# Performance work log

Measured on AMD Instinct MI355X. Metric: run time of the kernel, lower is better.

The kernel has to match this reference:

```python
import jax, jax.numpy as jnp
import numpy as np
from functools import partial

B, L, D = 4, 1024, 512
H = 8                 # attention heads
DIN = 2 * D           # mamba d_inner (expand=2)
N = 16                # mamba d_state
K = 4                 # mamba d_conv
R = 32                # dt_rank = ceil(D/16)


def setup_inputs() -> dict:
    key = jax.random.key(0)
    ks = jax.random.split(key, 24)
    s = 0.02
    nrm = lambda k, sh: (jax.random.normal(k, sh, dtype=jnp.float32) * s)
    inp = {
        'x':       jax.random.normal(ks[0], (B, L, D), dtype=jnp.float32),
        # attention projections
        'Wq': nrm(ks[1], (D, D)), 'bq': jnp.zeros((D,), jnp.float32),
        'Wk': nrm(ks[2], (D, D)), 'bk': jnp.zeros((D,), jnp.float32),
        'Wv': nrm(ks[3], (D, D)), 'bv': jnp.zeros((D,), jnp.float32),
        'Wo': nrm(ks[4], (D, D)), 'bo': jnp.zeros((D,), jnp.float32),
        # layernorms
        'ln1_g': jnp.ones((D,), jnp.float32), 'ln1_b': jnp.zeros((D,), jnp.float32),
        'ln2_g': jnp.ones((D,), jnp.float32), 'ln2_b': jnp.zeros((D,), jnp.float32),
        # mamba params
        'm_Win':   nrm(ks[5], (D, 2 * DIN)),            # in_proj (no bias)
        'm_conv_w': nrm(ks[6], (DIN, 1, K)),            # depthwise causal conv
        'm_conv_b': jnp.zeros((DIN,), jnp.float32),
        'm_Wx':    nrm(ks[7], (DIN, R + 2 * N)),        # x_proj (no bias)
        'm_Wdt':   nrm(ks[8], (R, DIN)),                # dt_proj
        'm_bdt':   jnp.full((DIN,), 0.5, jnp.float32),
        'm_Alog':  jnp.log(jnp.broadcast_to(jnp.arange(1, N + 1, dtype=jnp.float32), (DIN, N))).copy(),
        'm_D':     jnp.ones((DIN,), jnp.float32),
        'm_Wout':  nrm(ks[9], (DIN, D)),                # out_proj (no bias)
    }
    return inp


def _layernorm(x, g, b, eps=1e-5):
    mu = jnp.mean(x, axis=-1, keepdims=True)
    var = jnp.var(x, axis=-1, keepdims=True)
    return (x - mu) * jax.lax.rsqrt(var + eps) * g + b


def _mamba(x, Win, conv_w, conv_b, Wx, Wdt, bdt, Alog, Dp, Wout):
    b, l, _ = x.shape
    xz = x @ Win                           # [B,L,2*DIN]
    xi, z = xz[..., :DIN], xz[..., DIN:]
    # causal depthwise conv over time
    xt = jnp.transpose(xi, (0, 2, 1))      # [B,DIN,L]
    xt = jax.lax.conv_general_dilated(
        xt, conv_w, window_strides=(1,), padding=[(K - 1, 0)],
        feature_group_count=DIN, dimension_numbers=('NCH', 'OIH', 'NCH'))
    xc = jax.nn.silu(jnp.transpose(xt, (0, 2, 1)) + conv_b)   # [B,L,DIN]
    # input-dependent SSM params
    dbl = xc @ Wx                          # [B,L,R+2N]
    dt = jax.nn.softplus(dbl[..., :R] @ Wdt + bdt)            # [B,L,DIN]
    Bm = dbl[..., R:R + N]                 # [B,L,N]
    Cm = dbl[..., R + N:]                  # [B,L,N]
    A = -jnp.exp(Alog)                     # [DIN,N]
    dA = jnp.exp(dt[..., None] * A)                     # [B,L,DIN,N]
    dBx = (dt * xc)[..., None] * Bm[:, :, None, :]      # [B,L,DIN,N]

    def step(h, t):
        dA_t, dBx_t, C_t = t
        h = h * dA_t + dBx_t               # [B,DIN,N]
        y = jnp.einsum('bdn,bn->bd', h, C_t)
        return h, y

    h0 = jnp.zeros((b, DIN, N), xc.dtype)
    _, ys = jax.lax.scan(step, h0, (jnp.swapaxes(dA, 0, 1),
                                    jnp.swapaxes(dBx, 0, 1),
                                    jnp.swapaxes(Cm, 0, 1)))
    y = jnp.swapaxes(ys, 0, 1)             # [B,L,DIN]
    y = y + xc * Dp
    y = y * jax.nn.silu(z)
    return y @ Wout                        # [B,L,D]


def reference(x, Wq, bq, Wk, bk, Wv, bv, Wo, bo, ln1_g, ln1_b, ln2_g, ln2_b,
              m_Win, m_conv_w, m_conv_b, m_Wx, m_Wdt, m_bdt, m_Alog, m_D, m_Wout):
    b, l, d = x.shape
    E = d // H
    q = (x @ Wq + bq).reshape(b, l, H, E)
    k = (x @ Wk + bk).reshape(b, l, H, E)
    v = (x @ Wv + bv).reshape(b, l, H, E)
    scores = jnp.einsum('blhe,bshe->bhls', q, k) * (E ** -0.5)
    attn = jax.nn.softmax(scores, axis=-1)                    # [B,H,L,L]
    o = jnp.einsum('bhls,bshe->blhe', attn, v).reshape(b, l, d)
    new_x = o @ Wo + bo
    x1 = _layernorm(x + new_x, ln1_g, ln1_b)
    y = _mamba(x1, m_Win, m_conv_w, m_conv_b, m_Wx, m_Wdt, m_bdt, m_Alog, m_D, m_Wout)
    out = _layernorm(x1 + y, ln2_g, ln2_b)
    return out, attn
```

## Files before the change

### kernel.cpp

```cpp
#include <hip/hip_runtime.h>
#include <hip/hip_bf16.h>

#define BB 4
#define LL 1024
#define DD 512
#define HH 8
#define EE 64
#define DIN 1024
#define NN 16
#define KK 4
#define RR 32
#define BL (BB*LL)
#define CC 32
#define LC (LL/CC)
#define BDN (BB*DIN*NN)

using bf16 = __hip_bfloat16;
typedef __attribute__((ext_vector_type(8))) short short8;
typedef __attribute__((ext_vector_type(4))) float f32x4;

__device__ __forceinline__ float ldf(const float* p) { return *p; }
__device__ __forceinline__ float ldf(const bf16* p) { return __bfloat162float(*p); }
__device__ __forceinline__ void stf(float* p, float v) { *p = v; }
__device__ __forceinline__ void stf(bf16* p, float v) { *p = __float2bfloat16(v); }

__global__ void cvt_k(const float* __restrict__ in, bf16* __restrict__ out, int n)
{
    int i = blockIdx.x * 256 + threadIdx.x;
    if (i < n) out[i] = __float2bfloat16(in[i]);
}

struct TpwJob { const float* in; bf16* out; int Kd, Nd, gx, tile0; };
struct TpwJobs { TpwJob j[7]; };

__global__ void tpw_batch_k(TpwJobs jobs)
{
    const int tile = blockIdx.x;
    int ji = 0;
#pragma unroll
    for (int i = 1; i < 7; ++i) if (tile >= jobs.j[i].tile0) ji = i;
    const TpwJob jb = jobs.j[ji];
    const int lt = tile - jb.tile0;
    const int n0 = (lt % jb.gx) * 32;
    const int k0 = (lt / jb.gx) * 32;

    __shared__ float t[32][33];
    const int tx = threadIdx.x & 31, ty = threadIdx.x >> 5;
#pragma unroll
    for (int i = 0; i < 4; ++i)
        t[ty + 8 * i][tx] = jb.in[(size_t)(k0 + ty + 8 * i) * jb.Nd + n0 + tx];
    __syncthreads();
#pragma unroll
    for (int i = 0; i < 4; ++i)
        jb.out[(size_t)(n0 + ty + 8 * i) * jb.Kd + k0 + tx] = __float2bfloat16(t[tx][ty + 8 * i]);
}

__global__ void tpv_k(const bf16* __restrict__ v, bf16* __restrict__ vT)
{
    __shared__ float t[32][33];
    const int l0 = blockIdx.x * 32;
    const int e0 = blockIdx.y * 32;
    const int bh = blockIdx.z, b = bh >> 3, h = bh & 7;
    const int tx = threadIdx.x & 31, ty = threadIdx.x >> 5;
#pragma unroll
    for (int i = 0; i < 4; ++i)
        t[ty + 8 * i][tx] = ldf(&v[(size_t)(b * LL + l0 + ty + 8 * i) * DD + h * EE + e0 + tx]);
    __syncthreads();
#pragma unroll
    for (int i = 0; i < 4; ++i)
        stf(&vT[(size_t)(bh * EE + e0 + ty + 8 * i) * LL + l0 + tx], t[tx][ty + 8 * i]);
}

template <typename TC>
__global__ void mfma_gemm128_k(const bf16* __restrict__ A, int lda,
                               const bf16* __restrict__ Bt0, size_t bstride, int ldb,
                               const float* __restrict__ bias0,
                               const float* __restrict__ bias1,
                               const float* __restrict__ bias2,
                               TC* __restrict__ C0, size_t cstride, int ldc, int Kd)
{
    const int z = blockIdx.z;
    const bf16* Bt = Bt0 + (size_t)z * bstride;
    TC* C = C0 + (size_t)z * cstride;
    const float* bias = (z == 0) ? bias0 : (z == 1) ? bias1 : bias2;

    const int lane = threadIdx.x & 63;
    const int w = threadIdx.x >> 6;
    const int m = lane & 15, quad = lane >> 4;
    const int m0 = blockIdx.y * 128 + (w >> 1) * 64;
    const int n0 = blockIdx.x * 128 + (w & 1) * 64;

    f32x4 acc[4][4] = {};
    const bf16* ap = A + (size_t)(m0 + m) * lda + quad * 8;
    const bf16* bp = Bt + (size_t)(n0 + m) * ldb + quad * 8;
    const size_t rsa = (size_t)16 * lda;
    const size_t rsb = (size_t)16 * ldb;
    for (int k = 0; k < Kd; k += 32) {
        short8 a[4], b[4];
#pragma unroll
        for (int i = 0; i < 4; ++i) a[i] = *(const short8*)(ap + i * rsa + k);
#pragma unroll
        for (int j = 0; j < 4; ++j) b[j] = *(const short8*)(bp + j * rsb + k);
#pragma unroll
        for (int i = 0; i < 4; ++i)
#pragma unroll
            for (int j = 0; j < 4; ++j)
                acc[i][j] = __builtin_amdgcn_mfma_f32_16x16x32_bf16(a[i], b[j], acc[i][j], 0, 0, 0);
    }
    float bv[4];
#pragma unroll
    for (int j = 0; j < 4; ++j) bv[j] = bias ? bias[n0 + j * 16 + m] : 0.f;
#pragma unroll
    for (int i = 0; i < 4; ++i)
#pragma unroll
        for (int j = 0; j < 4; ++j)
#pragma unroll
            for (int r = 0; r < 4; ++r) {
                int row = m0 + i * 16 + quad * 4 + r;
                int col = n0 + j * 16 + m;
                stf(&C[(size_t)row * ldc + col], acc[i][j][r] + bv[j]);
            }
}

template <typename TC>
__global__ void mfma_gemm_k(const bf16* __restrict__ A, int lda,
                            const bf16* __restrict__ Bt, int ldb,
                            const float* __restrict__ bias,
                            TC* __restrict__ C, int ldc, int Kd)
{
    const int lane = threadIdx.x & 63;
    const int w = threadIdx.x >> 6;
    const int m = lane & 15, quad = lane >> 4;
    const int m0 = blockIdx.y * 64 + (w >> 1) * 32;
    const int n0 = blockIdx.x * 64 + (w & 1) * 32;
    f32x4 acc[2][2] = {};
    const bf16* a0p = A + (size_t)(m0 + m) * lda + quad * 8;
    const bf16* a1p = a0p + (size_t)16 * lda;
    const bf16* b0p = Bt + (size_t)(n0 + m) * ldb + quad * 8;
    const bf16* b1p = b0p + (size_t)16 * ldb;
    for (int k = 0; k < Kd; k += 32) {
        short8 a0 = *(const short8*)(a0p + k);
        short8 a1 = *(const short8*)(a1p + k);
        short8 b0 = *(const short8*)(b0p + k);
        short8 b1 = *(const short8*)(b1p + k);
        acc[0][0] = __builtin_amdgcn_mfma_f32_16x16x32_bf16(a0, b0, acc[0][0], 0, 0, 0);
        acc[0][1] = __builtin_amdgcn_mfma_f32_16x16x32_bf16(a0, b1, acc[0][1], 0, 0, 0);
        acc[1][0] = __builtin_amdgcn_mfma_f32_16x16x32_bf16(a1, b0, acc[1][0], 0, 0, 0);
        acc[1][1] = __builtin_amdgcn_mfma_f32_16x16x32_bf16(a1, b1, acc[1][1], 0, 0, 0);
    }
#pragma unroll
    for (int i = 0; i < 2; ++i)
#pragma unroll
        for (int j = 0; j < 2; ++j)
#pragma unroll
            for (int r = 0; r < 4; ++r) {
                int row = m0 + i * 16 + quad * 4 + r;
                int col = n0 + j * 16 + (lane & 15);
                float vv = acc[i][j][r] + (bias ? bias[col] : 0.f);
                stf(&C[(size_t)row * ldc + col], vv);
            }
}

__global__ void attn_fused_k(const bf16* __restrict__ q, const bf16* __restrict__ k,
                             const bf16* __restrict__ vT,
                             float* __restrict__ attn, bf16* __restrict__ o)
{
    const int rt = blockIdx.x;
    const int bh = blockIdx.y, b = bh >> 3, h = bh & 7;
    const int w = threadIdx.x >> 6;
    const int lane = threadIdx.x & 63;
    const int m = lane & 15, quad = lane >> 4;
    __shared__ float pm[4][16], ps[4][16];
    __shared__ bf16 P[16][1032];

    const bf16* qp = q + (size_t)(b * LL + rt * 16 + m) * DD + h * EE + quad * 8;
    short8 a0 = *(const short8*)(qp);
    short8 a1 = *(const short8*)(qp + 32);

    f32x4 acc[16];
#pragma unroll
    for (int t = 0; t < 16; ++t) {
        int srow = w * 256 + t * 16 + m;
        const bf16* kp = k + (size_t)(b * LL + srow) * DD + h * EE + quad * 8;
        short8 b0 = *(const short8*)(kp);
        short8 b1 = *(const short8*)(kp + 32);
        f32x4 c = {};
        c = __builtin_amdgcn_mfma_f32_16x16x32_bf16(a0, b0, c, 0, 0, 0);
        c = __builtin_amdgcn_mfma_f32_16x16x32_bf16(a1, b1, c, 0, 0, 0);
        acc[t] = c;
    }

#pragma unroll
    for (int r = 0; r < 4; ++r) {
        float mx = -1e30f;
#pragma unroll
        for (int t = 0; t < 16; ++t) { acc[t][r] *= 0.125f; mx = fmaxf(mx, acc[t][r]); }
        mx = fmaxf(mx, __shfl_xor(mx, 1)); mx = fmaxf(mx, __shfl_xor(mx, 2));
        mx = fmaxf(mx, __shfl_xor(mx, 4)); mx = fmaxf(mx, __shfl_xor(mx, 8));
        if (m == 0) pm[w][quad * 4 + r] = mx;
    }
    __syncthreads();
#pragma unroll
    for (int r = 0; r < 4; ++r) {
        float mx = fmaxf(fmaxf(pm[0][quad * 4 + r], pm[1][quad * 4 + r]),
                         fmaxf(pm[2][quad * 4 + r], pm[3][quad * 4 + r]));
        float s = 0.f;
#pragma unroll
        for (int t = 0; t < 16; ++t) { float e = __expf(acc[t][r] - mx); acc[t][r] = e; s += e; }
        s += __shfl_xor(s, 1); s += __shfl_xor(s, 2);
        s += __shfl_xor(s, 4); s += __shfl_xor(s, 8);
        if (m == 0) ps[w][quad * 4 + r] = s;
    }
    __syncthreads();
#pragma unroll
    for (int r = 0; r < 4; ++r) {
        float tot = ps[0][quad * 4 + r] + ps[1][quad * 4 + r] + ps[2][quad * 4 + r] + ps[3][quad * 4 + r];
        float inv = 1.f / tot;
        int row = rt * 16 + quad * 4 + r;
        float* op = attn + ((size_t)bh * LL + row) * LL + w * 256 + (lane & 15);
#pragma unroll
        for (int t = 0; t < 16; ++t) {
            float pv = acc[t][r] * inv;
            op[t * 16] = pv;
            P[quad * 4 + r][w * 256 + t * 16 + m] = __float2bfloat16(pv);
        }
    }
    __syncthreads();

    const bf16* vp = vT + (size_t)(bh * EE + w * 16 + m) * LL + quad * 8;
    f32x4 oacc = {};
    for (int k0 = 0; k0 < LL; k0 += 32) {
        short8 af = *(const short8*)(&P[m][k0 + quad * 8]);
        short8 bf = *(const short8*)(vp + k0);
        oacc = __builtin_amdgcn_mfma_f32_16x16x32_bf16(af, bf, oacc, 0, 0, 0);
    }
#pragma unroll
    for (int r = 0; r < 4; ++r) {
        int row = rt * 16 + quad * 4 + r;
        stf(&o[(size_t)(b * LL + row) * DD + h * EE + w * 16 + (lane & 15)], oacc[r]);
    }
}

template <typename TA, typename TC, bool SP>
__global__ void gemm_k(const TA* __restrict__ A, int lda,
                       const float* __restrict__ B, int ldb,
                       const float* __restrict__ bias,
                       TC* __restrict__ C, int ldc,
                       int M, int N, int Kd)
{
    __shared__ float As[32][33];
    __shared__ float Bs[32][33];
    const int tid = threadIdx.x;
    const int tx = tid & 31;
    const int ty = tid >> 5;
    const int rowBase = blockIdx.y * 32;
    const int colBase = blockIdx.x * 32;
    float acc[4] = {0.f, 0.f, 0.f, 0.f};

    for (int k0 = 0; k0 < Kd; k0 += 32) {
#pragma unroll
        for (int i = 0; i < 4; ++i) {
            int r = ty + 8 * i;
            As[r][tx] = ldf(&A[(size_t)(rowBase + r) * lda + k0 + tx]);
            Bs[r][tx] = B[(size_t)(k0 + r) * ldb + colBase + tx];
        }
        __syncthreads();
#pragma unroll 8
        for (int kk = 0; kk < 32; ++kk) {
            float bv = Bs[kk][tx];
#pragma unroll
            for (int i = 0; i < 4; ++i) acc[i] += As[ty + 8 * i][kk] * bv;
        }
        __syncthreads();
    }
#pragma unroll
    for (int i = 0; i < 4; ++i) {
        int row = rowBase + ty + 8 * i;
        int col = colBase + tx;
        float r = acc[i] + (bias ? bias[col] : 0.f);
        if (SP) r = (r > 20.f) ? r : log1pf(__expf(r));
        stf(&C[(size_t)row * ldc + col], r);
    }
}

template <typename TA, typename TR, typename TO>
__global__ void add_ln_k(const TA* __restrict__ a, const TR* __restrict__ r,
                         const float* __restrict__ g, const float* __restrict__ be,
                         TO* __restrict__ out)
{
    const int row = blockIdx.x;
    const int tid = threadIdx.x;
    __shared__ float red[256];
    const size_t base = (size_t)row * DD;
    float v0 = ldf(&a[base + tid]) + ldf(&r[base + tid]);
    float v1 = ldf(&a[base + 256 + tid]) + ldf(&r[base + 256 + tid]);
    red[tid] = v0 + v1;
    __syncthreads();
    for (int off = 128; off > 0; off >>= 1) {
        if (tid < off) red[tid] += red[tid + off];
        __syncthreads();
    }
    const float mu = red[0] * (1.f / 512.f);
    __syncthreads();
    float d0 = v0 - mu, d1 = v1 - mu;
    red[tid] = d0 * d0 + d1 * d1;
    __syncthreads();
    for (int off = 128; off > 0; off >>= 1) {
        if (tid < off) red[tid] += red[tid + off];
        __syncthreads();
    }
    const float rs = rsqrtf(red[0] * (1.f / 512.f) + 1e-5f);
    stf(&out[base + tid], d0 * rs * g[tid] + be[tid]);
    stf(&out[base + 256 + tid], d1 * rs * g[tid + 256] + be[tid + 256]);
}

__global__ void conv_silu_k(const bf16* __restrict__ xz,
                            const float* __restrict__ w,
                            const float* __restrict__ cb,
                            bf16* __restrict__ xc)
{
    const int idx = blockIdx.x * 256 + threadIdx.x;
    const int c = idx & (DIN - 1);
    const int t = (idx >> 10) & (LL - 1);
    const int b = idx >> 20;
    float acc = cb[c];
    const bf16* xi = xz + (size_t)b * LL * (2 * DIN) + c;
#pragma unroll
    for (int j = 0; j < KK; ++j) {
        int tt = t - (KK - 1) + j;
        if (tt >= 0) acc += w[c * KK + j] * ldf(&xi[(size_t)tt * (2 * DIN)]);
    }
    stf(&xc[idx], acc / (1.f + __expf(-acc)));
}

__global__ void scan_p1_k(const bf16* __restrict__ dt, const bf16* __restrict__ xc,
                          const float* __restrict__ dbl, const float* __restrict__ Alog,
                          float* __restrict__ P, float* __restrict__ S)
{
    const int d = (blockIdx.x & 3) * 256 + threadIdx.x;
    const int c = blockIdx.x >> 2;
    const int b = blockIdx.y;
    float A[NN];
#pragma unroll
    for (int n = 0; n < NN; ++n) A[n] = -__expf(Alog[d * NN + n]);
    const int t0 = c * LC;
    const bf16* dt_b = dt + ((size_t)b * LL + t0) * DIN + d;
    const bf16* xc_b = xc + ((size_t)b * LL + t0) * DIN + d;
    const float* dbl_b = dbl + ((size_t)b * LL + t0) * 64 + RR;
    float h[NN];
#pragma unroll
    for (int n = 0; n < NN; ++n) h[n] = 0.f;
    float sdt = 0.f;
#pragma unroll 4
    for (int t = 0; t < LC; ++t) {
        float dtv = ldf(&dt_b[(size_t)t * DIN]);
        float xcv = ldf(&xc_b[(size_t)t * DIN]);
        float dtx = dtv * xcv;
        sdt += dtv;
#pragma unroll
        for (int n = 0; n < NN; ++n) {
            float dA = __expf(dtv * A[n]);
            h[n] = h[n] * dA + dtx * dbl_b[(size_t)t * 64 + n];
        }
    }
    float* Pp = P + (size_t)c * BDN + ((size_t)(b * DIN + d)) * NN;
    float* Sp = S + (size_t)c * BDN + ((size_t)(b * DIN + d)) * NN;
#pragma unroll
    for (int n = 0; n < NN; ++n) { Pp[n] = __expf(sdt * A[n]); Sp[n] = h[n]; }
}

__global__ void scan_p2_k(const float* __restrict__ P, const float* __restrict__ S,
                          float* __restrict__ Hc)
{
    const size_t bdn = (size_t)blockIdx.x * 256 + threadIdx.x;
    float h = 0.f;
#pragma unroll
    for (int c = 0; c < CC; ++c) {
        Hc[(size_t)c * BDN + bdn] = h;
        h = S[(size_t)c * BDN + bdn] + P[(size_t)c * BDN + bdn] * h;
    }
}

__global__ void scan_p3_k(const bf16* __restrict__ dt, const bf16* __restrict__ xc,
                          const float* __restrict__ dbl, const float* __restrict__ Alog,
                          const float* __restrict__ Dv, const float* __restrict__ Hc,
                          bf16* __restrict__ xzm)
{
    const int d = (blockIdx.x & 3) * 256 + threadIdx.x;
    const int c = blockIdx.x >> 2;
    const int b = blockIdx.y;
    float A[NN];
#pragma unroll
    for (int n = 0; n < NN; ++n) A[n] = -__expf(Alog[d * NN + n]);
    const float Dp = Dv[d];
    const int t0 = c * LC;
    const bf16* dt_b = dt + ((size_t)b * LL + t0) * DIN + d;
    const bf16* xc_b = xc + ((size_t)b * LL + t0) * DIN + d;
    const float* dbl_b = dbl + ((size_t)b * LL + t0) * 64 + RR;
    bf16* xz_b = xzm + ((size_t)b * LL + t0) * (2 * DIN);
    const float* hp = Hc + (size_t)c * BDN + ((size_t)(b * DIN + d)) * NN;
    float h[NN];
#pragma unroll
    for (int n = 0; n < NN; ++n) h[n] = hp[n];
#pragma unroll 2
    for (int t = 0; t < LC; ++t) {
        float dtv = ldf(&dt_b[(size_t)t * DIN]);
        float xcv = ldf(&xc_b[(size_t)t * DIN]);
        float dtx = dtv * xcv;
        float y = 0.f;
#pragma unroll
        for (int n = 0; n < NN; ++n) {
            float dA = __expf(dtv * A[n]);
            h[n] = h[n] * dA + dtx * dbl_b[(size_t)t * 64 + n];
            y += h[n] * dbl_b[(size_t)t * 64 + NN + n];
        }
        float zv = ldf(&xz_b[(size_t)t * (2 * DIN) + DIN + d]);
        float yv = y + xcv * Dp;
        yv *= zv / (1.f + __expf(-zv));
        stf(&xz_b[(size_t)t * (2 * DIN) + d], yv);
    }
}

extern "C" void kernel_launch(void* const* d_in, const int* in_sizes, int n_in,
                              void* d_out, int out_size, void* d_ws, size_t ws_size,
                              hipStream_t stream)
{
    const float* x    = (const float*)d_in[0];
    const float* Wq   = (const float*)d_in[1];
    const float* bq   = (const float*)d_in[2];
    const float* Wk   = (const float*)d_in[3];
    const float* bk   = (const float*)d_in[4];
    const float* Wv   = (const float*)d_in[5];
    const float* bv   = (const float*)d_in[6];
    const float* Wo   = (const float*)d_in[7];
    const float* bo   = (const float*)d_in[8];
    const float* g1   = (const float*)d_in[9];
    const float* b1   = (const float*)d_in[10];
    const float* g2   = (const float*)d_in[11];
    const float* b2   = (const float*)d_in[12];
    const float* Win  = (const float*)d_in[13];
    const float* cw   = (const float*)d_in[14];
    const float* cb   = (const float*)d_in[15];
    const float* Wx   = (const float*)d_in[16];
    const float* Wdt  = (const float*)d_in[17];
    const float* bdt  = (const float*)d_in[18];
    const float* Alog = (const float*)d_in[19];
    const float* Dv   = (const float*)d_in[20];
    const float* Wout = (const float*)d_in[21];

    float* out  = (float*)d_out;
    float* attn = out + (size_t)BL * DD;

    const size_t M1 = 1048576;
    bf16* wsb = (bf16*)d_ws;
    bf16* xb   = wsb;
    bf16* q    = wsb + 2*M1;
    bf16* kb   = wsb + 4*M1;
    bf16* v    = wsb + 6*M1;
    bf16* o    = wsb + 8*M1;
    bf16* x1   = wsb + 10*M1;
    bf16* xz   = wsb + 12*M1;
    bf16* xc   = wsb + 20*M1;
    bf16* dtb  = wsb + 24*M1;
    float* dbl = (float*)(wsb + 28*M1);
    bf16* vT   = wsb + 28*M1 + 524288;
    bf16* Wqt  = vT + 2*M1;
    bf16* Wkt  = Wqt + 262144;
    bf16* Wvt  = Wkt + 262144;
    bf16* Wot  = Wvt + 262144;
    bf16* Wint = Wot + 262144;
    bf16* Wxt  = Wint + M1;
    bf16* Woutt= Wxt + 65536;
    bf16* newx = q;
    bf16* ym   = v;
    float* Pp = (float*)xb;
    float* Sp = (float*)kb;
    float* Hc = (float*)vT;

    const dim3 blk(256);

    cvt_k<<<dim3(BL*DD/256), blk, 0, stream>>>(x, xb, BL*DD);
    TpwJobs tj;
    int t0 = 0, nj = 0;
    auto addjob = [&](const float* in, bf16* outp, int Kd, int Nd) {
        tj.j[nj] = {in, outp, Kd, Nd, Nd / 32, t0};
        t0 += (Nd / 32) * (Kd / 32);
        ++nj;
    };
    addjob(Wq,   Wqt,   DD,  DD);
    addjob(Wk,   Wkt,   DD,  DD);
    addjob(Wv,   Wvt,   DD,  DD);
    addjob(Wo,   Wot,   DD,  DD);
    addjob(Win,  Wint,  DD,  2*DIN);
    addjob(Wx,   Wxt,   DIN, 64);
    addjob(Wout, Woutt, DIN, DD);
    tpw_batch_k<<<dim3(t0), blk, 0, stream>>>(tj);

    mfma_gemm128_k<bf16><<<dim3(DD/128, BL/128, 3), blk, 0, stream>>>(
        xb, DD, Wqt, (size_t)DD*DD, DD, bq, bk, bv, q, (size_t)2*M1, DD, DD);
    tpv_k<<<dim3(LL/32, EE/32, BB*HH), blk, 0, stream>>>(v, vT);

    attn_fused_k<<<dim3(LL/16, BB*HH), blk, 0, stream>>>(q, kb, vT, attn, o);

    mfma_gemm128_k<bf16><<<dim3(DD/128, BL/128, 1), blk, 0, stream>>>(
        o, DD, Wot, 0, DD, bo, nullptr, nullptr, newx, 0, DD, DD);
    add_ln_k<float, bf16, bf16><<<dim3(BL), blk, 0, stream>>>(x, newx, g1, b1, x1);

    mfma_gemm128_k<bf16><<<dim3(2*DIN/128, BL/128, 1), blk, 0, stream>>>(
        x1, DD, Wint, 0, DD, nullptr, nullptr, nullptr, xz, 0, 2*DIN, DD);

    conv_silu_k<<<dim3(BL*DIN/256), blk, 0, stream>>>(xz, cw, cb, xc);

    mfma_gemm_k<float><<<dim3(64/64, BL/64), blk, 0, stream>>>(xc, DIN, Wxt, DIN, nullptr, dbl, 64, DIN);

    gemm_k<float, bf16, true><<<dim3(DIN/32, BL/32), blk, 0, stream>>>(dbl, 64, Wdt, DIN, bdt, dtb, DIN, BL, DIN, RR);

    scan_p1_k<<<dim3((DIN/256)*CC, BB), blk, 0, stream>>>(dtb, xc, dbl, Alog, Pp, Sp);
    scan_p2_k<<<dim3(BDN/256), blk, 0, stream>>>(Pp, Sp, Hc);
    scan_p3_k<<<dim3((DIN/256)*CC, BB), blk, 0, stream>>>(dtb, xc, dbl, Alog, Dv, Hc, xz);

    mfma_gemm128_k<bf16><<<dim3(DD/128, BL/128, 1), blk, 0, stream>>>(
        xz, 2*DIN, Woutt, 0, DIN, nullptr, nullptr, nullptr, ym, 0, DD, DIN);

    add_ln_k<bf16, bf16, float><<<dim3(BL), blk, 0, stream>>>(x1, ym, g2, b2, out);
}
```

Before: 517.5 us.

## Merge softmax reductions, halve attention LDS buffer, remap grid for locality

The fused attention kernel now computes each wave's local max and sum in one pass and combines them with an online-softmax rescale, which removes one block barrier. The bf16 probability staging buffer in LDS is halved by filling it in two phases: waves 0-1 write first, the PV MFMA runs over that half, then waves 2-3 write the second half. The grid is flattened and remapped so that consecutive blocks cycle over heads within a batch. This is meant to improve cache locality and, through the lower LDS use, occupancy. The cost is two extra barriers around the second half and some added exp work.

```diff
diff --git a/kernel.cpp b/kernel.cpp
--- a/kernel.cpp
+++ b/kernel.cpp
@@ -165,13 +165,15 @@
                              const bf16* __restrict__ vT,
                              float* __restrict__ attn, bf16* __restrict__ o)
 {
-    const int rt = blockIdx.x;
-    const int bh = blockIdx.y, b = bh >> 3, h = bh & 7;
+    const int n = blockIdx.x;
+    const int bh = ((n >> 9) << 3) | (n & 7);
+    const int rt = (n >> 3) & 63;
+    const int b = bh >> 3, h = bh & 7;
     const int w = threadIdx.x >> 6;
     const int lane = threadIdx.x & 63;
     const int m = lane & 15, quad = lane >> 4;
     __shared__ float pm[4][16], ps[4][16];
-    __shared__ bf16 P[16][1032];
+    __shared__ bf16 P[16][524];
 
     const bf16* qp = q + (size_t)(b * LL + rt * 16 + m) * DD + h * EE + quad * 8;
     short8 a0 = *(const short8*)(qp);
@@ -197,47 +199,66 @@
         for (int t = 0; t < 16; ++t) { acc[t][r] *= 0.125f; mx = fmaxf(mx, acc[t][r]); }
         mx = fmaxf(mx, __shfl_xor(mx, 1)); mx = fmaxf(mx, __shfl_xor(mx, 2));
         mx = fmaxf(mx, __shfl_xor(mx, 4)); mx = fmaxf(mx, __shfl_xor(mx, 8));
-        if (m == 0) pm[w][quad * 4 + r] = mx;
-    }
-    __syncthreads();
-#pragma unroll
-    for (int r = 0; r < 4; ++r) {
-        float mx = fmaxf(fmaxf(pm[0][quad * 4 + r], pm[1][quad * 4 + r]),
-                         fmaxf(pm[2][quad * 4 + r], pm[3][quad * 4 + r]));
         float s = 0.f;
 #pragma unroll
         for (int t = 0; t < 16; ++t) { float e = __expf(acc[t][r] - mx); acc[t][r] = e; s += e; }
         s += __shfl_xor(s, 1); s += __shfl_xor(s, 2);
         s += __shfl_xor(s, 4); s += __shfl_xor(s, 8);
-        if (m == 0) ps[w][quad * 4 + r] = s;
-    }
-    __syncthreads();
+        if (m == 0) { pm[w][quad * 4 + r] = mx; ps[w][quad * 4 + r] = s; }
+    }
+    __syncthreads();
+
+    float sc[4];
 #pragma unroll
     for (int r = 0; r < 4; ++r) {
-        float tot = ps[0][quad * 4 + r] + ps[1][quad * 4 + r] + ps[2][quad * 4 + r] + ps[3][quad * 4 + r];
-        float inv = 1.f / tot;
-        int row = rt * 16 + quad * 4 + r;
-        float* op = attn + ((size_t)bh * LL + row) * LL + w * 256 + (lane & 15);
+        const int row = quad * 4 + r;
+        float m0 = pm[0][row], m1 = pm[1][row], m2 = pm[2][row], m3 = pm[3][row];
+        float M = fmaxf(fmaxf(m0, m1), fmaxf(m2, m3));
+        float e0 = __expf(m0 - M), e1 = __expf(m1 - M), e2 = __expf(m2 - M), e3 = __expf(m3 - M);
+        float T = ps[0][row] * e0 + ps[1][row] * e1 + ps[2][row] * e2 + ps[3][row] * e3;
+        float ew = (w == 0) ? e0 : (w == 1) ? e1 : (w == 2) ? e2 : e3;
+        sc[r] = ew / T;
+    }
+#pragma unroll
+    for (int r = 0; r < 4; ++r) {
+        const int row = quad * 4 + r;
+        float* op = attn + ((size_t)bh * LL + rt * 16 + row) * LL + w * 256 + m;
 #pragma unroll
         for (int t = 0; t < 16; ++t) {
-            float pv = acc[t][r] * inv;
+            float pv = acc[t][r] * sc[r];
             op[t * 16] = pv;
-            P[quad * 4 + r][w * 256 + t * 16 + m] = __float2bfloat16(pv);
+            if (w < 2) P[row][(w & 1) * 256 + t * 16 + m] = __float2bfloat16(pv);
         }
     }
     __syncthreads();
 
     const bf16* vp = vT + (size_t)(bh * EE + w * 16 + m) * LL + quad * 8;
     f32x4 oacc = {};
-    for (int k0 = 0; k0 < LL; k0 += 32) {
+    for (int k0 = 0; k0 < 512; k0 += 32) {
         short8 af = *(const short8*)(&P[m][k0 + quad * 8]);
         short8 bf = *(const short8*)(vp + k0);
         oacc = __builtin_amdgcn_mfma_f32_16x16x32_bf16(af, bf, oacc, 0, 0, 0);
     }
+    __syncthreads();
+    if (w >= 2) {
+#pragma unroll
+        for (int r = 0; r < 4; ++r) {
+            const int row = quad * 4 + r;
+#pragma unroll
+            for (int t = 0; t < 16; ++t)
+                P[row][(w & 1) * 256 + t * 16 + m] = __float2bfloat16(acc[t][r] * sc[r]);
+        }
+    }
+    __syncthreads();
+    for (int k0 = 512; k0 < 1024; k0 += 32) {
+        short8 af = *(const short8*)(&P[m][k0 - 512 + quad * 8]);
+        short8 bf = *(const short8*)(vp + k0);
+        oacc = __builtin_amdgcn_mfma_f32_16x16x32_bf16(af, bf, oacc, 0, 0, 0);
+    }
 #pragma unroll
     for (int r = 0; r < 4; ++r) {
         int row = rt * 16 + quad * 4 + r;
-        stf(&o[(size_t)(b * LL + row) * DD + h * EE + w * 16 + (lane & 15)], oacc[r]);
+        stf(&o[(size_t)(b * LL + row) * DD + h * EE + w * 16 + m], oacc[r]);
     }
 }
 
@@ -500,7 +521,7 @@
         xb, DD, Wqt, (size_t)DD*DD, DD, bq, bk, bv, q, (size_t)2*M1, DD, DD);
     tpv_k<<<dim3(LL/32, EE/32, BB*HH), blk, 0, stream>>>(v, vT);
 
-    attn_fused_k<<<dim3(LL/16, BB*HH), blk, 0, stream>>>(q, kb, vT, attn, o);
+    attn_fused_k<<<dim3((LL/16)*BB*HH), blk, 0, stream>>>(q, kb, vT, attn, o);
 
     mfma_gemm128_k<bf16><<<dim3(DD/128, BL/128, 1), blk, 0, stream>>>(
         o, DD, Wot, 0, DD, bo, nullptr, nullptr, newx, 0, DD, DD);
```

Measured after the change: 519.4 us. No clear change (+0.4%).
